# Kernel optimization log

Measured on AMD Instinct MI355X. Metric: run time of the kernel, lower is better.

## Reference

```python
import jax, jax.numpy as jnp
import numpy as np

B, S, D, H = 2, 2048, 256, 8

def setup_inputs() -> dict:
    key = jax.random.key(0)
    ks = jax.random.split(key, 7)
    inputs = jax.random.normal(ks[0], (B, S, D), dtype=jnp.float32)
    timestamp = jnp.sort(jax.random.randint(ks[1], (B, S), 0, 100000, dtype=jnp.int32), axis=-1)
    wQ = jax.random.normal(ks[2], (H, D, D), dtype=jnp.float32) * 0.05
    wK = jax.random.normal(ks[3], (H, D, D), dtype=jnp.float32) * 0.05
    wV = jax.random.normal(ks[4], (H, D, D), dtype=jnp.float32) * 0.05
    wO = jax.random.normal(ks[5], (H * D, D), dtype=jnp.float32) * 0.05
    theta = jax.random.uniform(ks[6], (1, 1), dtype=jnp.float32)
    return {"inputs": inputs, "timestamp": timestamp, "wQ": wQ, "wK": wK,
            "wV": wV, "wO": wO, "theta": theta}

def reference(inputs, timestamp, wQ, wK, wV, wO, theta):
    b, s, d = inputs.shape
    # per-head projections (original loops over heads via TensorArray; vectorized here)
    Q = jnp.einsum('bsd,hde->bhse', inputs, wQ)
    K = jnp.einsum('bsd,hde->bhse', inputs, wK)
    V = jnp.einsum('bsd,hde->bhse', inputs, wV)
    exp_x = jnp.einsum('bhsd,bhtd->bhst', Q, K) / jnp.sqrt(jnp.float32(d))  # [B,H,S,S]
    x = jax.nn.softmax(exp_x, axis=-1)
    low_tri = jnp.tril(jnp.ones((s, s), dtype=jnp.float32))
    x = x * low_tri
    x = x / jnp.sum(x, axis=-1, keepdims=True)  # causal renormalized softmax

    # time-decay double-softmax branch. NOTE: the original module computes `a`
    # but returns x @ V, so `a`/`s_`/`d_` do not affect the output (dead code,
    # reproduced here for fidelity; XLA will DCE it).
    ts = timestamp.astype(jnp.float32)
    d_t = ts[:, None, :, None] - ts[:, None, None, :]  # diag(t) - t : [B,1,S,S]
    decay = (1.0 - jnp.cumsum(x, axis=-1)) * d_t * low_tri
    s_ = exp_x * jnp.exp(-(theta[0, 0] * theta[0, 0]) * decay)
    a = jax.nn.softmax(s_, axis=-1) * low_tri
    a = a / jnp.sum(a, axis=-1, keepdims=True)
    del a  # unused in original output

    ret = jnp.einsum('bhst,bhtd->bhsd', x, V)          # [B,H,S,D]
    out = ret.transpose(0, 2, 1, 3).reshape(b, s, -1)  # concat heads -> [B,S,H*D]
    return out @ wO
```

## Files before the change

kernel.cpp:

```cpp
#include <hip/hip_runtime.h>
#include <cstdint>
#include <cstddef>

#define S_LEN 2048
#define DIM   256
#define NH    8
#define NB    2
#define HDIM  (NH * DIM)

using bf16 = __bf16;
typedef __bf16 bf16x8 __attribute__((ext_vector_type(8)));
typedef __bf16 bf16x4 __attribute__((ext_vector_type(4)));
typedef float  f32x4  __attribute__((ext_vector_type(4)));

typedef const __attribute__((address_space(1))) unsigned int* as1_u32p;
typedef __attribute__((address_space(3))) unsigned int* as3_u32p;

__device__ __forceinline__ void cp16(const bf16* g, bf16* l) {
    __builtin_amdgcn_global_load_lds((as1_u32p)g, (as3_u32p)l, 16, 0, 0);
}


__global__ __launch_bounds__(256) void cast_x_kernel(const float* __restrict__ in,
                                                     bf16* __restrict__ out) {
    int i = (blockIdx.x * 256 + threadIdx.x) * 4;
    float4 v = *(const float4*)(in + i);
    bf16x4 o;
    o[0] = (bf16)v.x; o[1] = (bf16)v.y; o[2] = (bf16)v.z; o[3] = (bf16)v.w;
    *(bf16x4*)(out + i) = o;
}

__global__ __launch_bounds__(256) void transpose_w3_kernel(const float* __restrict__ wQ,
                                                           const float* __restrict__ wK,
                                                           const float* __restrict__ wV,
                                                           bf16* __restrict__ WQt,
                                                           bf16* __restrict__ WKt,
                                                           bf16* __restrict__ WVt) {
    __shared__ float tile[64][65];
    const int z   = blockIdx.z;
    const int mat = z >> 3;
    const int h   = z & 7;
    const float* in = (mat == 0 ? wQ : mat == 1 ? wK : wV) + (size_t)h * DIM * DIM;
    bf16* out       = (mat == 0 ? WQt : mat == 1 ? WKt : WVt) + (size_t)h * DIM * DIM;
    const int c0 = blockIdx.x * 64, r0 = blockIdx.y * 64;
    const int tr  = threadIdx.x >> 4;
    const int tc4 = (threadIdx.x & 15) * 4;
    #pragma unroll
    for (int p = 0; p < 4; ++p) {
        int row = p * 16 + tr;
        float4 v = *(const float4*)(in + (size_t)(r0 + row) * DIM + c0 + tc4);
        tile[row][tc4+0] = v.x; tile[row][tc4+1] = v.y;
        tile[row][tc4+2] = v.z; tile[row][tc4+3] = v.w;
    }
    __syncthreads();
    #pragma unroll
    for (int p = 0; p < 4; ++p) {
        int orow = p * 16 + tr;
        bf16x4 o;
        #pragma unroll
        for (int j = 0; j < 4; ++j) o[j] = (bf16)tile[tc4 + j][orow];
        *(bf16x4*)(out + (size_t)(c0 + orow) * DIM + r0 + tc4) = o;
    }
}

__global__ __launch_bounds__(256) void transpose_cast_kernel(const float* __restrict__ in,
                                                             bf16* __restrict__ out,
                                                             int R, int C) {
    __shared__ float tile[64][65];
    const int c0 = blockIdx.x * 64, r0 = blockIdx.y * 64;
    const int tr  = threadIdx.x >> 4;
    const int tc4 = (threadIdx.x & 15) * 4;
    #pragma unroll
    for (int p = 0; p < 4; ++p) {
        int row = p * 16 + tr;
        float4 v = *(const float4*)(in + (size_t)(r0 + row) * C + c0 + tc4);
        tile[row][tc4+0] = v.x; tile[row][tc4+1] = v.y;
        tile[row][tc4+2] = v.z; tile[row][tc4+3] = v.w;
    }
    __syncthreads();
    #pragma unroll
    for (int p = 0; p < 4; ++p) {
        int orow = p * 16 + tr;
        bf16x4 o;
        #pragma unroll
        for (int j = 0; j < 4; ++j) o[j] = (bf16)tile[tc4 + j][orow];
        *(bf16x4*)(out + (size_t)(c0 + orow) * R + r0 + tc4) = o;
    }
}

template<int EPI>
__device__ __forceinline__ void gemm_tile(const bf16* __restrict__ A, const bf16* __restrict__ BT,
                                          void* __restrict__ C, bf16* As, bf16* Bs,
                                          int tm, int tn, int K, int lda, int ldb, int ldc)
{
    const int tid  = threadIdx.x;
    const int lane = tid & 63;
    const int wave = tid >> 6;
    const int wm   = (wave >> 1) << 6;
    const int wn   = (wave & 1) << 6;
    const int l16  = lane & 15;
    const int quad = lane >> 4;

    const int m0 = tm << 7, n0 = tn << 7;

    const int srow = (lane >> 2);
    const int gch  = (lane & 3) ^ (srow & 3);

    f32x4 acc[4][4] = {};

    const int ksteps = K >> 5;

    #pragma unroll
    for (int j = 0; j < 2; ++j) {
        const int g = wave*2 + j;
        cp16(A  + (size_t)(m0 + g*16 + srow)*lda + (gch << 3), As + g*512);
        cp16(BT + (size_t)(n0 + g*16 + srow)*ldb + (gch << 3), Bs + g*512);
    }

    for (int ks = 0; ks < ksteps; ++ks) {
        const int pb = ks & 1;
        asm volatile("s_waitcnt vmcnt(0)" ::: "memory");
        __syncthreads();
        if (ks + 1 < ksteps) {
            const int k1 = (ks + 1) << 5;
            #pragma unroll
            for (int j = 0; j < 2; ++j) {
                const int g = wave*2 + j;
                cp16(A  + (size_t)(m0 + g*16 + srow)*lda + k1 + (gch << 3),
                     As + (pb ^ 1)*4096 + g*512);
                cp16(BT + (size_t)(n0 + g*16 + srow)*ldb + k1 + (gch << 3),
                     Bs + (pb ^ 1)*4096 + g*512);
            }
        }
        const bf16* Ab = As + pb*4096;
        const bf16* Bb = Bs + pb*4096;
        bf16x8 af[4], bfv[4];
        #pragma unroll
        for (int i = 0; i < 4; ++i) {
            const int row = wm + i*16 + l16;
            af[i]  = *(const bf16x8*)(Ab + row*32 + ((quad ^ (l16 & 3)) << 3));
        }
        #pragma unroll
        for (int i = 0; i < 4; ++i) {
            const int row = wn + i*16 + l16;
            bfv[i] = *(const bf16x8*)(Bb + row*32 + ((quad ^ (l16 & 3)) << 3));
        }
        #pragma unroll
        for (int i = 0; i < 4; ++i)
            #pragma unroll
            for (int j = 0; j < 4; ++j)
                acc[i][j] = __builtin_amdgcn_mfma_f32_16x16x32_bf16(af[i], bfv[j], acc[i][j], 0, 0, 0);
    }

    #pragma unroll
    for (int i = 0; i < 4; ++i)
        #pragma unroll
        for (int j = 0; j < 4; ++j)
            #pragma unroll
            for (int r = 0; r < 4; ++r) {
                int mg = m0 + wm + i*16 + quad*4 + r;
                int ng = n0 + wn + j*16 + l16;
                float v = acc[i][j][r];
                if (EPI == 0)      ((bf16*)C)[(size_t)mg * ldc + ng] = (bf16)v;
                else if (EPI == 1) ((float*)C)[(size_t)mg * ldc + ng] = v;
                else               atomicAdd(&((float*)C)[(size_t)mg * ldc + ng], v);
            }
}

__global__ __launch_bounds__(256) void proj_kernel(const bf16* __restrict__ Xb,
    const bf16* __restrict__ WQt, const bf16* __restrict__ WKt, const bf16* __restrict__ WVt,
    bf16* __restrict__ Qg, bf16* __restrict__ Kg, bf16* __restrict__ VTg)
{
    __shared__ __align__(16) bf16 smem[4 * 4096];
    const int by  = blockIdx.y;
    const int mat = by >> 4;
    const int b   = (by >> 3) & 1;
    const int h   = by & 7;
    const int bx  = blockIdx.x;
    const bf16*  Xbb = Xb + (size_t)b * S_LEN * DIM;
    const size_t bh  = (size_t)(b * NH + h);
    if (mat == 0) {
        gemm_tile<0>(Xbb, WQt + (size_t)h*DIM*DIM, Qg + bh*S_LEN*DIM, smem, smem + 8192,
                     bx & 15, bx >> 4, DIM, DIM, DIM, DIM);
    } else if (mat == 1) {
        gemm_tile<0>(Xbb, WKt + (size_t)h*DIM*DIM, Kg + bh*S_LEN*DIM, smem, smem + 8192,
                     bx & 15, bx >> 4, DIM, DIM, DIM, DIM);
    } else {
        gemm_tile<0>(WVt + (size_t)h*DIM*DIM, Xbb, VTg + bh*DIM*S_LEN, smem, smem + 8192,
                     bx & 1, bx >> 1, DIM, DIM, DIM, S_LEN);
    }
}

__global__ __launch_bounds__(256) void outproj_kernel(const bf16* __restrict__ Ret,
                                                      const bf16* __restrict__ WOt,
                                                      float* __restrict__ out)
{
    __shared__ __align__(16) bf16 smem[4 * 4096];
    int bx = blockIdx.x;
    int t  = bx & 63;
    int kq = bx >> 6;
    gemm_tile<2>(Ret + kq*512, WOt + kq*512, out, smem, smem + 8192,
                 t >> 1, t & 1, 512, HDIM, HDIM, DIM);
}

__global__ __launch_bounds__(256) void attn_kernel(const bf16* __restrict__ Qg,
                                                   const bf16* __restrict__ Kg,
                                                   const bf16* __restrict__ VTg,
                                                   bf16* __restrict__ Ret,
                                                   bf16* __restrict__ Opart,
                                                   float* __restrict__ Lpart)
{
    __shared__ __align__(16) bf16 KsB[2][32 * 256];
    __shared__ __align__(16) bf16 VTs[256 * 32];
    __shared__ __align__(16) bf16 Ps [4 * 16 * 40];

    const int tid  = threadIdx.x;
    const int lane = tid & 63;
    const int wave = tid >> 6;
    const int l16  = lane & 15;
    const int quad = lane >> 4;

    const int bx = blockIdx.x;
    const int R  = (bx < 256) ? bx : (bx < 512 ? 767 - bx : bx);
    const int bh = R & 15;
    const int r  = R >> 4;
    int qt, s; bool split;
    if (r < 40) {
        const int g = r / 5, j = r % 5;
        if (j == 0)      { qt = 15 - g;     split = false; s = 0; }
        else if (j <= 2) { qt = 31 - 2*g;   split = true;  s = j - 1; }
        else             { qt = 30 - 2*g;   split = true;  s = j - 3; }
    } else { qt = 47 - r; split = false; s = 0; }
    const int b = bh >> 3, h = bh & 7;

    int kstep0, kstep1;
    if (split) { kstep0 = s * (qt + 1); kstep1 = kstep0 + qt + 1; }
    else       { kstep0 = 0;           kstep1 = 2*qt + 2; }

    const bf16* Qbh  = Qg  + (size_t)(b*NH + h) * S_LEN * DIM;
    const bf16* Kbh  = Kg  + (size_t)(b*NH + h) * S_LEN * DIM;
    const bf16* VTbh = VTg + (size_t)(b*NH + h) * DIM * S_LEN;

    const int qbase = qt * 64 + wave * 16;

    bf16x8 qf[8];
    #pragma unroll
    for (int kc = 0; kc < 8; ++kc)
        qf[kc] = *(const bf16x8*)(Qbh + (size_t)(qbase + l16)*DIM + kc*32 + quad*8);

    f32x4 o[16] = {};
    float l_part[4] = {0.f, 0.f, 0.f, 0.f};

    {
        const int t00 = kstep0 << 5;
        #pragma unroll
        for (int j = 0; j < 4; ++j) {
            const int sN = (((wave << 2) + j) << 6) + lane;
            const int ts = sN >> 5, cs = sN & 31;
            cp16(Kbh + (size_t)(t00 + ts)*DIM + ((cs ^ ts) << 3),
                 &KsB[0][0] + (((wave << 2) + j) << 9));
        }
    }

    for (int step = kstep0; step < kstep1; ++step) {
        const int pb = (step - kstep0) & 1;
        asm volatile("s_waitcnt vmcnt(0)\n\ts_barrier" ::: "memory");

        const int t0 = step << 5;
        #pragma unroll
        for (int j = 0; j < 4; ++j) {
            const int sN = (((wave << 2) + j) << 6) + lane;
            const int es = sN >> 2, cs = sN & 3;
            cp16(VTbh + (size_t)es*S_LEN + t0 + ((cs ^ ((es >> 1) & 3)) << 3),
                 &VTs[0] + (((wave << 2) + j) << 9));
        }
        const bool havek = (step + 1 < kstep1);
        if (havek) {
            const int t1 = (step + 1) << 5;
            #pragma unroll
            for (int j = 0; j < 4; ++j) {
                const int sN = (((wave << 2) + j) << 6) + lane;
                const int ts = sN >> 5, cs = sN & 31;
                cp16(Kbh + (size_t)(t1 + ts)*DIM + ((cs ^ ts) << 3),
                     &KsB[pb ^ 1][0] + (((wave << 2) + j) << 9));
            }
        }

        const bf16* KsP = &KsB[pb][0];

        f32x4 sacc[2] = {};
        #pragma unroll
        for (int kc = 0; kc < 8; ++kc) {
            const int ch = (kc << 2) + quad;
            bf16x8 b0 = *(const bf16x8*)(KsP + (l16 << 8)        + ((ch ^ l16) << 3));
            bf16x8 b1 = *(const bf16x8*)(KsP + ((16 + l16) << 8) + ((ch ^ (16 + l16)) << 3));
            sacc[0] = __builtin_amdgcn_mfma_f32_16x16x32_bf16(qf[kc], b0, sacc[0], 0,0,0);
            sacc[1] = __builtin_amdgcn_mfma_f32_16x16x32_bf16(qf[kc], b1, sacc[1], 0,0,0);
        }

        float pv[2][4];
        #pragma unroll
        for (int r2 = 0; r2 < 4; ++r2) {
            const int qgi = qbase + quad*4 + r2;
            const bool ok0 = (t0 + l16)      <= qgi;
            const bool ok1 = (t0 + 16 + l16) <= qgi;
            float p0 = ok0 ? __expf(sacc[0][r2] * 0.0625f) : 0.0f;
            float p1 = ok1 ? __expf(sacc[1][r2] * 0.0625f) : 0.0f;
            l_part[r2] += p0 + p1;
            pv[0][r2] = p0; pv[1][r2] = p1;
        }

        #pragma unroll
        for (int nt = 0; nt < 2; ++nt)
            #pragma unroll
            for (int r2 = 0; r2 < 4; ++r2)
                Ps[wave*640 + (quad*4 + r2)*40 + nt*16 + l16] = (bf16)pv[nt][r2];

        if (havek) asm volatile("s_waitcnt vmcnt(4)\n\ts_barrier" ::: "memory");
        else       asm volatile("s_waitcnt vmcnt(0)\n\ts_barrier" ::: "memory");

        bf16x8 pf = *(const bf16x8*)(Ps + wave*640 + l16*40 + quad*8);
        #pragma unroll
        for (int ct = 0; ct < 16; ++ct) {
            const int e = (ct << 4) + l16;
            bf16x8 vf = *(const bf16x8*)(&VTs[0] + (e << 5) + ((quad ^ ((e >> 1) & 3)) << 3));
            o[ct] = __builtin_amdgcn_mfma_f32_16x16x32_bf16(pf, vf, o[ct], 0,0,0);
        }
    }

    float lsum[4];
    #pragma unroll
    for (int r2 = 0; r2 < 4; ++r2) {
        float l = l_part[r2];
        l += __shfl_xor(l, 1);
        l += __shfl_xor(l, 2);
        l += __shfl_xor(l, 4);
        l += __shfl_xor(l, 8);
        lsum[r2] = l;
    }

    if (!split) {
        #pragma unroll
        for (int r2 = 0; r2 < 4; ++r2) {
            const int qgi = qbase + quad*4 + r2;
            const float inv = 1.0f / lsum[r2];
            #pragma unroll
            for (int ct = 0; ct < 16; ++ct)
                Ret[((size_t)b*S_LEN + qgi)*HDIM + h*DIM + ct*16 + l16] = (bf16)(o[ct][r2] * inv);
        }
    } else {
        const size_t slot = ((size_t)(bh*16 + (qt - 16)))*2 + s;
        bf16*  Ob = Opart + slot * (64*256);
        float* Lb = Lpart + slot * 64;
        #pragma unroll
        for (int r2 = 0; r2 < 4; ++r2) {
            const int trow = wave*16 + quad*4 + r2;
            #pragma unroll
            for (int ct = 0; ct < 16; ++ct)
                Ob[(size_t)trow*256 + ct*16 + l16] = (bf16)o[ct][r2];
            if (l16 == 0) Lb[trow] = lsum[r2];
        }
    }
}

__global__ __launch_bounds__(256) void combine_kernel(const bf16* __restrict__ Opart,
                                                      const float* __restrict__ Lpart,
                                                      bf16* __restrict__ Ret)
{
    const int bx  = blockIdx.x;
    const int bh  = bx >> 4;
    const int qti = bx & 15;
    const int b = bh >> 3, h = bh & 7;
    const int row  = threadIdx.x >> 2;
    const int col0 = (threadIdx.x & 3) * 64;

    const size_t slot0 = ((size_t)(bh*16 + qti))*2;
    const bf16* O0 = Opart + slot0 * (64*256) + (size_t)row*256 + col0;
    const bf16* O1 = O0 + 64*256;
    const float inv = 1.0f / (Lpart[slot0*64 + row] + Lpart[(slot0+1)*64 + row]);

    const int q = (qti + 16)*64 + row;
    bf16* dst = Ret + ((size_t)b*S_LEN + q)*HDIM + h*DIM + col0;
    #pragma unroll
    for (int ch = 0; ch < 8; ++ch) {
        bf16x8 a = *(const bf16x8*)(O0 + ch*8);
        bf16x8 c = *(const bf16x8*)(O1 + ch*8);
        bf16x8 w;
        #pragma unroll
        for (int j = 0; j < 8; ++j) w[j] = (bf16)(((float)a[j] + (float)c[j]) * inv);
        *(bf16x8*)(dst + ch*8) = w;
    }
}


extern "C" void kernel_launch(void* const* d_in, const int* in_sizes, int n_in,
                              void* d_out, int out_size, void* d_ws, size_t ws_size,
                              hipStream_t stream)
{
    (void)in_sizes; (void)n_in; (void)ws_size;
    const float* X  = (const float*)d_in[0];
    const float* wQ = (const float*)d_in[2];
    const float* wK = (const float*)d_in[3];
    const float* wV = (const float*)d_in[4];
    const float* wO = (const float*)d_in[5];

    char* ws = (char*)d_ws;
    const size_t MB = 1u << 20;
    bf16*  Xb    = (bf16*)(ws + 0*MB);
    bf16*  WQt   = (bf16*)(ws + 2*MB);
    bf16*  WKt   = (bf16*)(ws + 3*MB);
    bf16*  WVt   = (bf16*)(ws + 4*MB);
    bf16*  WOt   = (bf16*)(ws + 5*MB);
    bf16*  Qg    = (bf16*)(ws + 6*MB);
    bf16*  Kg    = (bf16*)(ws + 22*MB);
    bf16*  VTg   = (bf16*)(ws + 38*MB);
    bf16*  Ret   = (bf16*)(ws + 54*MB);
    bf16*  Opart = (bf16*)(ws + 70*MB);
    float* Lpart = (float*)(ws + 86*MB);

    hipMemsetAsync(d_out, 0, (size_t)out_size * sizeof(float), stream);

    cast_x_kernel        <<<1024, 256, 0, stream>>>(X, Xb);
    transpose_w3_kernel  <<<dim3(4, 4, 24), 256, 0, stream>>>(wQ, wK, wV, WQt, WKt, WVt);
    transpose_cast_kernel<<<dim3(4, 32),    256, 0, stream>>>(wO, WOt, HDIM, DIM);
    proj_kernel    <<<dim3(32, 48), 256, 0, stream>>>(Xb, WQt, WKt, WVt, Qg, Kg, VTg);
    attn_kernel    <<<768,          256, 0, stream>>>(Qg, Kg, VTg, Ret, Opart, Lpart);
    combine_kernel <<<256,          256, 0, stream>>>(Opart, Lpart, Ret);
    outproj_kernel <<<256,          256, 0, stream>>>(Ret, WOt, (float*)d_out);
}
```

Before: 192.7 us.

## Fuse prep kernels and rebalance causal attention with 1/2/3-way key splits

Merges the X cast and the three weight transpose kernels into one launch. The causal attention work is repartitioned so short query tiles run unsplit, middle tiles split their key range in two and long tiles split it in three. Blocks are issued in a hand-ordered sequence so the largest pieces start first. The combine kernel now reduces a variable number of partial results. This targets the tail imbalance and the launch overhead, at the cost of more partial-output traffic and a larger combine pass.

```diff
diff --git a/kernel.cpp b/kernel.cpp
--- a/kernel.cpp
+++ b/kernel.cpp
@@ -20,54 +20,41 @@
     __builtin_amdgcn_global_load_lds((as1_u32p)g, (as3_u32p)l, 16, 0, 0);
 }
 
-
-__global__ __launch_bounds__(256) void cast_x_kernel(const float* __restrict__ in,
-                                                     bf16* __restrict__ out) {
-    int i = (blockIdx.x * 256 + threadIdx.x) * 4;
-    float4 v = *(const float4*)(in + i);
-    bf16x4 o;
-    o[0] = (bf16)v.x; o[1] = (bf16)v.y; o[2] = (bf16)v.z; o[3] = (bf16)v.w;
-    *(bf16x4*)(out + i) = o;
-}
-
-__global__ __launch_bounds__(256) void transpose_w3_kernel(const float* __restrict__ wQ,
-                                                           const float* __restrict__ wK,
-                                                           const float* __restrict__ wV,
-                                                           bf16* __restrict__ WQt,
-                                                           bf16* __restrict__ WKt,
-                                                           bf16* __restrict__ WVt) {
+__global__ __launch_bounds__(256) void prep_kernel(const float* __restrict__ X,
+                                                   const float* __restrict__ wQ,
+                                                   const float* __restrict__ wK,
+                                                   const float* __restrict__ wV,
+                                                   const float* __restrict__ wO,
+                                                   bf16* __restrict__ Xb,
+                                                   bf16* __restrict__ WQt,
+                                                   bf16* __restrict__ WKt,
+                                                   bf16* __restrict__ WVt,
+                                                   bf16* __restrict__ WOt)
+{
+    const int z = blockIdx.z;
+    if (z == 4) {
+        const int t = (blockIdx.y*4 + blockIdx.x)*256 + threadIdx.x;
+        #pragma unroll
+        for (int p = 0; p < 8; ++p) {
+            const int i = (t + p*32768)*4;
+            float4 v = *(const float4*)(X + i);
+            bf16x4 o;
+            o[0] = (bf16)v.x; o[1] = (bf16)v.y; o[2] = (bf16)v.z; o[3] = (bf16)v.w;
+            *(bf16x4*)(Xb + i) = o;
+        }
+        return;
+    }
     __shared__ float tile[64][65];
-    const int z   = blockIdx.z;
-    const int mat = z >> 3;
-    const int h   = z & 7;
-    const float* in = (mat == 0 ? wQ : mat == 1 ? wK : wV) + (size_t)h * DIM * DIM;
-    bf16* out       = (mat == 0 ? WQt : mat == 1 ? WKt : WVt) + (size_t)h * DIM * DIM;
-    const int c0 = blockIdx.x * 64, r0 = blockIdx.y * 64;
-    const int tr  = threadIdx.x >> 4;
-    const int tc4 = (threadIdx.x & 15) * 4;
-    #pragma unroll
-    for (int p = 0; p < 4; ++p) {
-        int row = p * 16 + tr;
-        float4 v = *(const float4*)(in + (size_t)(r0 + row) * DIM + c0 + tc4);
-        tile[row][tc4+0] = v.x; tile[row][tc4+1] = v.y;
-        tile[row][tc4+2] = v.z; tile[row][tc4+3] = v.w;
-    }
-    __syncthreads();
-    #pragma unroll
-    for (int p = 0; p < 4; ++p) {
-        int orow = p * 16 + tr;
-        bf16x4 o;
-        #pragma unroll
-        for (int j = 0; j < 4; ++j) o[j] = (bf16)tile[tc4 + j][orow];
-        *(bf16x4*)(out + (size_t)(c0 + orow) * DIM + r0 + tc4) = o;
-    }
-}
-
-__global__ __launch_bounds__(256) void transpose_cast_kernel(const float* __restrict__ in,
-                                                             bf16* __restrict__ out,
-                                                             int R, int C) {
-    __shared__ float tile[64][65];
-    const int c0 = blockIdx.x * 64, r0 = blockIdx.y * 64;
+    const float* in; bf16* out; int R, C, r0, c0;
+    if (z < 3) {
+        const int h = blockIdx.y >> 2;
+        in  = (z == 0 ? wQ : z == 1 ? wK : wV) + (size_t)h * DIM * DIM;
+        out = (z == 0 ? WQt : z == 1 ? WKt : WVt) + (size_t)h * DIM * DIM;
+        R = DIM; C = DIM; r0 = (blockIdx.y & 3) * 64; c0 = blockIdx.x * 64;
+    } else {
+        in = wO; out = WOt; R = HDIM; C = DIM;
+        r0 = blockIdx.y * 64; c0 = blockIdx.x * 64;
+    }
     const int tr  = threadIdx.x >> 4;
     const int tc4 = (threadIdx.x & 15) * 4;
     #pragma unroll
@@ -214,28 +201,35 @@
     __shared__ __align__(16) bf16 VTs[256 * 32];
     __shared__ __align__(16) bf16 Ps [4 * 16 * 40];
 
+    static const unsigned char order[63] = {
+        10,31,32,60, 29,30,57,58,61,62, 9,27,28,51,54,55,56,59,
+        25,26,48,49,52,53, 8,23,24,42,45,46,47,50, 21,22,39,40,43,44,
+        7,19,20,33,36,37,38,41, 17,18,34,35, 6,15,16, 13,14, 5,11,12,
+        4,3,2,1,0 };
+
     const int tid  = threadIdx.x;
     const int lane = tid & 63;
     const int wave = tid >> 6;
     const int l16  = lane & 15;
     const int quad = lane >> 4;
 
-    const int bx = blockIdx.x;
-    const int R  = (bx < 256) ? bx : (bx < 512 ? 767 - bx : bx);
-    const int bh = R & 15;
-    const int r  = R >> 4;
-    int qt, s; bool split;
-    if (r < 40) {
-        const int g = r / 5, j = r % 5;
-        if (j == 0)      { qt = 15 - g;     split = false; s = 0; }
-        else if (j <= 2) { qt = 31 - 2*g;   split = true;  s = j - 1; }
-        else             { qt = 30 - 2*g;   split = true;  s = j - 3; }
-    } else { qt = 47 - r; split = false; s = 0; }
+    const int bx  = blockIdx.x;
+    const int bh  = bx & 15;
+    const int bid = order[bx >> 4];
+    int qt, s, nsp;
+    if (bid <= 10)      { qt = bid;              s = 0;       nsp = 1; }
+    else if (bid <= 32) { int k = bid - 11; qt = 11 + (k >> 1); s = k & 1; nsp = 2; }
+    else                { int k = bid - 33; int q3 = k / 3; qt = 22 + q3; s = k - 3*q3; nsp = 3; }
     const int b = bh >> 3, h = bh & 7;
 
     int kstep0, kstep1;
-    if (split) { kstep0 = s * (qt + 1); kstep1 = kstep0 + qt + 1; }
-    else       { kstep0 = 0;           kstep1 = 2*qt + 2; }
+    if (nsp == 1)      { kstep0 = 0; kstep1 = 2*qt + 2; }
+    else if (nsp == 2) { kstep0 = s*(qt + 1); kstep1 = kstep0 + qt + 1; }
+    else {
+        const int S2 = 2*qt + 2, base = S2/3, rem = S2 - 3*base;
+        kstep0 = s*base + (s < rem ? s : rem);
+        kstep1 = kstep0 + base + (s < rem ? 1 : 0);
+    }
 
     const bf16* Qbh  = Qg  + (size_t)(b*NH + h) * S_LEN * DIM;
     const bf16* Kbh  = Kg  + (size_t)(b*NH + h) * S_LEN * DIM;
@@ -339,7 +333,7 @@
         lsum[r2] = l;
     }
 
-    if (!split) {
+    if (nsp == 1) {
         #pragma unroll
         for (int r2 = 0; r2 < 4; ++r2) {
             const int qgi = qbase + quad*4 + r2;
@@ -349,7 +343,8 @@
                 Ret[((size_t)b*S_LEN + qgi)*HDIM + h*DIM + ct*16 + l16] = (bf16)(o[ct][r2] * inv);
         }
     } else {
-        const size_t slot = ((size_t)(bh*16 + (qt - 16)))*2 + s;
+        const int slotbase = (qt <= 21) ? ((qt - 11)*2 + s) : (22 + (qt - 22)*3 + s);
+        const size_t slot = (size_t)bh*52 + slotbase;
         bf16*  Ob = Opart + slot * (64*256);
         float* Lb = Lpart + slot * 64;
         #pragma unroll
@@ -367,27 +362,35 @@
                                                       const float* __restrict__ Lpart,
                                                       bf16* __restrict__ Ret)
 {
-    const int bx  = blockIdx.x;
-    const int bh  = bx >> 4;
-    const int qti = bx & 15;
+    const int bx = blockIdx.x;
+    const int bh = bx / 21;
+    const int ti = bx - bh*21;
+    const int qt = 11 + ti;
+    const int n  = (qt <= 21) ? 2 : 3;
+    const int slotbase = (qt <= 21) ? (qt - 11)*2 : (22 + (qt - 22)*3);
+    const size_t slot0 = (size_t)bh*52 + slotbase;
     const int b = bh >> 3, h = bh & 7;
     const int row  = threadIdx.x >> 2;
     const int col0 = (threadIdx.x & 3) * 64;
 
-    const size_t slot0 = ((size_t)(bh*16 + qti))*2;
+    float l = 0.f;
+    for (int i = 0; i < n; ++i) l += Lpart[(slot0 + i)*64 + row];
+    const float inv = 1.0f / l;
+
     const bf16* O0 = Opart + slot0 * (64*256) + (size_t)row*256 + col0;
-    const bf16* O1 = O0 + 64*256;
-    const float inv = 1.0f / (Lpart[slot0*64 + row] + Lpart[(slot0+1)*64 + row]);
-
-    const int q = (qti + 16)*64 + row;
+    const int q = qt*64 + row;
     bf16* dst = Ret + ((size_t)b*S_LEN + q)*HDIM + h*DIM + col0;
     #pragma unroll
     for (int ch = 0; ch < 8; ++ch) {
-        bf16x8 a = *(const bf16x8*)(O0 + ch*8);
-        bf16x8 c = *(const bf16x8*)(O1 + ch*8);
+        float acc[8] = {};
+        for (int i = 0; i < n; ++i) {
+            bf16x8 a = *(const bf16x8*)(O0 + (size_t)i*(64*256) + ch*8);
+            #pragma unroll
+            for (int j = 0; j < 8; ++j) acc[j] += (float)a[j];
+        }
         bf16x8 w;
         #pragma unroll
-        for (int j = 0; j < 8; ++j) w[j] = (bf16)(((float)a[j] + (float)c[j]) * inv);
+        for (int j = 0; j < 8; ++j) w[j] = (bf16)(acc[j] * inv);
         *(bf16x8*)(dst + ch*8) = w;
     }
 }
@@ -416,15 +419,14 @@
     bf16*  VTg   = (bf16*)(ws + 38*MB);
     bf16*  Ret   = (bf16*)(ws + 54*MB);
     bf16*  Opart = (bf16*)(ws + 70*MB);
-    float* Lpart = (float*)(ws + 86*MB);
+    float* Lpart = (float*)(ws + 98*MB);
 
     hipMemsetAsync(d_out, 0, (size_t)out_size * sizeof(float), stream);
 
-    cast_x_kernel        <<<1024, 256, 0, stream>>>(X, Xb);
-    transpose_w3_kernel  <<<dim3(4, 4, 24), 256, 0, stream>>>(wQ, wK, wV, WQt, WKt, WVt);
-    transpose_cast_kernel<<<dim3(4, 32),    256, 0, stream>>>(wO, WOt, HDIM, DIM);
+    prep_kernel    <<<dim3(4, 32, 5), 256, 0, stream>>>(X, wQ, wK, wV, wO,
+                                                        Xb, WQt, WKt, WVt, WOt);
     proj_kernel    <<<dim3(32, 48), 256, 0, stream>>>(Xb, WQt, WKt, WVt, Qg, Kg, VTg);
-    attn_kernel    <<<768,          256, 0, stream>>>(Qg, Kg, VTg, Ret, Opart, Lpart);
-    combine_kernel <<<256,          256, 0, stream>>>(Opart, Lpart, Ret);
+    attn_kernel    <<<1008,         256, 0, stream>>>(Qg, Kg, VTg, Ret, Opart, Lpart);
+    combine_kernel <<<336,          256, 0, stream>>>(Opart, Lpart, Ret);
     outproj_kernel <<<256,          256, 0, stream>>>(Ret, WOt, (float*)d_out);
 }
```

Result: slower. 198.0 us (+2.7%).
